# Performance work log

Hardware: AMD Instinct MI355X
Metric: run time of the kernel (lower is better)

Reference implementation:

```python
import jax, jax.numpy as jnp
import numpy as np

INCH, OUTCH, H, W = 1536, 256, 60, 60
B = 4


def resize_bilinear_align_corners(x, oh, ow):
    """F.interpolate(x, (oh, ow), mode='bilinear', align_corners=True) for NCHW x."""
    Bx, C, Hx, Wx = x.shape
    ys = jnp.linspace(0.0, Hx - 1.0, oh)
    xs = jnp.linspace(0.0, Wx - 1.0, ow)
    y0 = jnp.floor(ys).astype(jnp.int32)
    x0 = jnp.floor(xs).astype(jnp.int32)
    y1 = jnp.minimum(y0 + 1, Hx - 1)
    x1 = jnp.minimum(x0 + 1, Wx - 1)
    wy = (ys - y0.astype(x.dtype))[:, None]   # [oh,1]
    wx = (xs - x0.astype(x.dtype))[None, :]   # [1,ow]
    g = lambda yi, xi: x[:, :, yi][:, :, :, xi]  # [B,C,oh,ow]
    top = (1.0 - wx) * g(y0, x0) + wx * g(y0, x1)
    bot = (1.0 - wx) * g(y1, x0) + wx * g(y1, x1)
    return (1.0 - wy) * top + wy * bot


def setup_inputs() -> dict:
    key = jax.random.key(0)
    ks = jax.random.split(key, 8)
    feat_supp = jax.random.normal(ks[0], (B, INCH, H, W), dtype=jnp.float32)
    feat_query = jax.random.normal(ks[1], (B, INCH, H, W), dtype=jnp.float32)
    mask_supp = jax.random.uniform(ks[2], (B, 1, 473, 473), dtype=jnp.float32)
    scale = 0.02
    W_lpf = jax.random.normal(ks[3], (OUTCH, INCH), dtype=jnp.float32) * scale   # shared_LPF 1x1 conv
    W_supp = jax.random.normal(ks[4], (OUTCH, INCH), dtype=jnp.float32) * scale  # supp_linear
    W_query = jax.random.normal(ks[5], (OUTCH, INCH), dtype=jnp.float32) * scale # query_linear
    W_final = jax.random.normal(ks[6], (OUTCH, 2 * OUTCH), dtype=jnp.float32) * scale
    b_final = jax.random.normal(ks[7], (OUTCH,), dtype=jnp.float32) * scale
    return {"feat_supp": feat_supp, "feat_query": feat_query, "mask_supp": mask_supp,
            "W_lpf": W_lpf, "W_supp": W_supp, "W_query": W_query,
            "W_final": W_final, "b_final": b_final}


def conv1x1(x, Wm):
    # x: [b,c,h,w], Wm: [o,c]
    return jnp.einsum('bchw,oc->bohw', x, Wm)


def reference(feat_supp, feat_query, mask_supp, W_lpf, W_supp, W_query, W_final, b_final):
    b, d, h, w = feat_supp.shape
    hw = h * w
    v_supp = conv1x1(feat_supp, W_lpf)    # [b,256,h,w]
    v_query = conv1x1(feat_query, W_lpf)  # [b,256,h,w]
    k = conv1x1(feat_supp, W_supp).transpose(0, 2, 3, 1).reshape(b, hw, -1)   # [b,hw,256]
    q = conv1x1(feat_query, W_query).transpose(0, 2, 3, 1).reshape(b, hw, -1) # [b,hw,256]
    attn = jnp.einsum('bqd,bkd->bqk', q, k)  # [b,hw,hw]
    fg_mask = resize_bilinear_align_corners(mask_supp, h, w)  # [b,1,h,w]
    bg_suppress = ((1.0 - fg_mask) * -999.0).reshape(b, 1, hw)
    attn = jax.nn.softmax(attn + bg_suppress, axis=-1)
    vs = v_supp.transpose(0, 2, 3, 1).reshape(b, hw, -1)      # [b,hw,256]
    out = jnp.einsum('bqk,bkd->bqd', attn, vs)                # [b,hw,256]
    out = out.reshape(b, h, w, -1).transpose(0, 3, 1, 2)      # [b,256,h,w]
    cat = jnp.concatenate([out, v_query], axis=1)             # [b,512,h,w]
    final = jax.nn.relu(conv1x1(cat, W_final) + b_final[None, :, None, None])
    return final, attn.reshape(b, h, w, h, w)
```

## Files before the change

kernel.cpp:

```cpp
#include <hip/hip_runtime.h>
#include <stdint.h>

typedef unsigned short u16;
typedef _Float16 h16;
typedef __attribute__((ext_vector_type(4))) float f32x4;
typedef __attribute__((ext_vector_type(8))) short s16x8;
typedef __attribute__((ext_vector_type(8))) _Float16 h16x8;
typedef __attribute__((ext_vector_type(4))) _Float16 h16x4;
typedef __attribute__((ext_vector_type(4))) unsigned short u16x4;
typedef __attribute__((ext_vector_type(8))) unsigned short u16x8;

#define HW   3600
#define HWP  3648
#define DIM  256
#define CIN  1536
#define LDK  72
#define NCB  58
#define PSH  15.0f

__device__ __forceinline__ u16 f2bf(float f) {
  uint32_t u = __float_as_uint(f);
  uint32_t r = (u + 0x7fffu + ((u >> 16) & 1u)) >> 16;
  return (u16)r;
}
__device__ __forceinline__ float bf2f(u16 h) { return __uint_as_float((uint32_t)h << 16); }

template<int MR, int NR>
__device__ __forceinline__ void mfma_tile(const h16 (*As)[LDK], const h16 (*Bs)[LDK],
                                          int lane, int wr, int wc, f32x4 acc[MR][NR]) {
#pragma unroll
  for (int ks = 0; ks < 2; ++ks) {
    const int ko = ks * 32 + ((lane >> 4) << 3);
    h16x8 af[MR], bv[NR];
#pragma unroll
    for (int m = 0; m < MR; ++m) af[m] = *(const h16x8*)&As[wr + m * 16 + (lane & 15)][ko];
#pragma unroll
    for (int n = 0; n < NR; ++n) bv[n] = *(const h16x8*)&Bs[wc + n * 16 + (lane & 15)][ko];
#pragma unroll
    for (int m = 0; m < MR; ++m)
#pragma unroll
      for (int n = 0; n < NR; ++n)
        acc[m][n] = __builtin_amdgcn_mfma_f32_16x16x32_f16(af[m], bv[n], acc[m][n], 0, 0, 0);
  }
}

template<int MR, int NR>
__device__ __forceinline__ void mfma_tile_bf(const u16 (*As)[LDK], const u16 (*Bs)[LDK],
                                             int lane, int wr, int wc, f32x4 acc[MR][NR]) {
#pragma unroll
  for (int ks = 0; ks < 2; ++ks) {
    const int ko = ks * 32 + ((lane >> 4) << 3);
    s16x8 af[MR], bv[NR];
#pragma unroll
    for (int m = 0; m < MR; ++m) af[m] = *(const s16x8*)&As[wr + m * 16 + (lane & 15)][ko];
#pragma unroll
    for (int n = 0; n < NR; ++n) bv[n] = *(const s16x8*)&Bs[wc + n * 16 + (lane & 15)][ko];
#pragma unroll
    for (int m = 0; m < MR; ++m)
#pragma unroll
      for (int n = 0; n < NR; ++n)
        acc[m][n] = __builtin_amdgcn_mfma_f32_16x16x32_bf16(af[m], bv[n], acc[m][n], 0, 0, 0);
  }
}

#define NW    (256 * 1536)
#define NWF   (256 * 512)
#define NPAD  (4 * 256 * 48)
#define NPREP (14400 + 3 * NW + NWF + NPAD)

__global__ __launch_bounds__(256) void k_prep(
    const float* __restrict__ mask, const float* __restrict__ Wlpf,
    const float* __restrict__ Wsupp, const float* __restrict__ Wquery,
    const float* __restrict__ Wfin,
    float* __restrict__ sup, h16* __restrict__ Wl16, h16* __restrict__ Ws16,
    h16* __restrict__ Wq16, h16* __restrict__ Wf16, u16* __restrict__ vs) {
  int i = blockIdx.x * 256 + threadIdx.x;
  if (i < 14400) {
    int b = i / HW, p = i % HW, py = p / 60, px = p % 60;
    float fg = mask[(size_t)b * 473 * 473 + (size_t)(py * 8) * 473 + px * 8];
    sup[i] = (1.0f - fg) * -999.0f;
  } else if (i < 14400 + NW) {
    int j = i - 14400; Wl16[j] = (h16)Wlpf[j];
  } else if (i < 14400 + 2 * NW) {
    int j = i - 14400 - NW; Ws16[j] = (h16)Wsupp[j];
  } else if (i < 14400 + 3 * NW) {
    int j = i - 14400 - 2 * NW; Wq16[j] = (h16)Wquery[j];
  } else if (i < 14400 + 3 * NW + NWF) {
    int j = i - 14400 - 3 * NW; Wf16[j] = (h16)Wfin[j];
  } else if (i < NPREP) {
    int j = i - 14400 - 3 * NW - NWF;
    int b = j / (256 * 48), rem = j % (256 * 48), d = rem / 48, kk = rem % 48;
    vs[((size_t)b * DIM + d) * HWP + 3600 + kk] = 0;
  }
}

__global__ __launch_bounds__(256) void k_conv(
    const h16* __restrict__ Wl16, const h16* __restrict__ Ws16, const h16* __restrict__ Wq16,
    const float* __restrict__ featS, const float* __restrict__ featQ,
    u16* __restrict__ vs, h16* __restrict__ vq,
    h16* __restrict__ kbuf, h16* __restrict__ qbuf) {
  const int lin = blockIdx.x;
  const int xcd = lin & 7, slot = lin >> 3;
  const int ct = slot >> 2, rb = slot & 3;
  const int b = xcd & 3, isQ = xcd >> 2;
  const int rowBase = rb * 128;
  const int colBase = ct * 128;
  const int tid = threadIdx.x, lane = tid & 63, wid = tid >> 6;
  const int wr = (wid >> 1) << 6, wc = (wid & 1) << 6;
  const bool isV = rowBase < 256;
  const h16* Wbase = isV ? (Wl16 + (size_t)rowBase * CIN)
                         : ((isQ ? Wq16 : Ws16) + (size_t)(rowBase - 256) * CIN);
  const float* feat = (isQ ? featQ : featS) + (size_t)b * CIN * HW;

  __shared__ h16 As[128][LDK];
  __shared__ h16 Bs[128][LDK];
  f32x4 acc[4][4] = {};

  const int a_r = tid >> 3, a_kv = (tid & 7) << 3;
  const int b_n = tid & 127, b_kh = (tid >> 7) << 5;
  const int gnc = colBase + b_n;
  const int gn = gnc < HW ? gnc : HW - 1;

  s16x8 aR[4];
  float bR[32];
#pragma unroll
  for (int i = 0; i < 4; ++i)
    aR[i] = *(const s16x8*)&Wbase[(size_t)(a_r + i * 32) * CIN + a_kv];
#pragma unroll
  for (int g = 0; g < 8; ++g) {
    const float* s = feat + (size_t)(b_kh + g * 4) * HW + gn;
#pragma unroll
    for (int c = 0; c < 4; ++c) bR[g * 4 + c] = s[(size_t)c * HW];
  }

  for (int kt = 0; kt < 24; ++kt) {
#pragma unroll
    for (int i = 0; i < 4; ++i) *(s16x8*)&As[a_r + i * 32][a_kv] = aR[i];
#pragma unroll
    for (int g = 0; g < 8; ++g) {
      h16x4 h = {(h16)bR[g * 4], (h16)bR[g * 4 + 1], (h16)bR[g * 4 + 2], (h16)bR[g * 4 + 3]};
      *(h16x4*)&Bs[b_n][b_kh + g * 4] = h;
    }
    if (kt < 23) {
      const int k0n = (kt + 1) * 64;
#pragma unroll
      for (int i = 0; i < 4; ++i)
        aR[i] = *(const s16x8*)&Wbase[(size_t)(a_r + i * 32) * CIN + k0n + a_kv];
#pragma unroll
      for (int g = 0; g < 8; ++g) {
        const float* s = feat + (size_t)(k0n + b_kh + g * 4) * HW + gn;
#pragma unroll
        for (int c = 0; c < 4; ++c) bR[g * 4 + c] = s[(size_t)c * HW];
      }
    }
    __syncthreads();
    mfma_tile<4, 4>(As, Bs, lane, wr, wc, acc);
    __syncthreads();
  }

  if (isV && !isQ) {
    u16* dst = vs + (size_t)b * DIM * HWP;
#pragma unroll
    for (int m = 0; m < 4; ++m) {
      const int d0 = rowBase + wr + m * 16 + ((lane >> 4) << 2);
#pragma unroll
      for (int n = 0; n < 4; ++n) {
        const int pix = colBase + wc + n * 16 + (lane & 15);
        if (pix < HW) {
#pragma unroll
          for (int r = 0; r < 4; ++r) dst[(size_t)(d0 + r) * HWP + pix] = f2bf(acc[m][n][r]);
        }
      }
    }
  } else {
    h16* dst = (isV ? vq : (isQ ? qbuf : kbuf)) + (size_t)b * HW * DIM;
    const int dOff = isV ? 0 : -256;
#pragma unroll
    for (int m = 0; m < 4; ++m) {
      const int d0 = rowBase + wr + m * 16 + ((lane >> 4) << 2) + dOff;
#pragma unroll
      for (int n = 0; n < 4; ++n) {
        const int pix = colBase + wc + n * 16 + (lane & 15);
        if (pix < HW) {
          h16x4 h = {(h16)acc[m][n][0], (h16)acc[m][n][1],
                     (h16)acc[m][n][2], (h16)acc[m][n][3]};
          *(h16x4*)&dst[(size_t)pix * DIM + d0] = h;
        }
      }
    }
  }
}

__global__ __launch_bounds__(256) void k_qk(
    const h16* __restrict__ qbuf, const h16* __restrict__ kbuf,
    const float* __restrict__ sup, u16* __restrict__ p, float* __restrict__ stat) {
  const int hwid = blockIdx.x;
  const int xcd = hwid & 7, pos = hwid >> 3;
  const int logical = (xcd < 4) ? xcd * 421 + pos : 1684 + (xcd - 4) * 420 + pos;
  const int b = logical / 841, rem = logical % 841;
  const int rt = rem / 29, ct = rem % 29;
  const int rowBase = rt * 128, colBase = ct * 128;
  const int tid = threadIdx.x, lane = tid & 63, wid = tid >> 6;
  const int wr = (wid >> 1) << 6, wc = (wid & 1) << 6;
  const h16* Aq = qbuf + (size_t)b * HW * DIM;
  const h16* Bk = kbuf + (size_t)b * HW * DIM;

  __shared__ __align__(16) char smem[128 * LDK * 2 * 2];
  h16 (*As)[LDK] = (h16(*)[LDK])smem;
  h16 (*Bs)[LDK] = (h16(*)[LDK])(smem + 128 * LDK * 2);
  u16 (*pC)[136] = (u16(*)[136])smem;

  f32x4 acc[4][4] = {};
  const int r0 = tid >> 3, kv8 = (tid & 7) << 3;

  int gaR[4], gbR[4];
#pragma unroll
  for (int i = 0; i < 4; ++i) {
    const int r = r0 + i * 32;
    int ga = rowBase + r; gaR[i] = ga < HW ? ga : HW - 1;
    int gb = colBase + r; gbR[i] = gb < HW ? gb : HW - 1;
  }
  s16x8 aR[4], bR[4];
#pragma unroll
  for (int i = 0; i < 4; ++i) {
    aR[i] = *(const s16x8*)(Aq + (size_t)gaR[i] * DIM + kv8);
    bR[i] = *(const s16x8*)(Bk + (size_t)gbR[i] * DIM + kv8);
  }

  for (int kt = 0; kt < 4; ++kt) {
#pragma unroll
    for (int i = 0; i < 4; ++i) {
      *(s16x8*)&As[r0 + i * 32][kv8] = aR[i];
      *(s16x8*)&Bs[r0 + i * 32][kv8] = bR[i];
    }
    if (kt < 3) {
      const int k0n = (kt + 1) * 64;
#pragma unroll
      for (int i = 0; i < 4; ++i) {
        aR[i] = *(const s16x8*)(Aq + (size_t)gaR[i] * DIM + k0n + kv8);
        bR[i] = *(const s16x8*)(Bk + (size_t)gbR[i] * DIM + k0n + kv8);
      }
    }
    __syncthreads();
    mfma_tile<4, 4>(As, Bs, lane, wr, wc, acc);
    __syncthreads();
  }

  float sup4[4]; int kp4[4];
#pragma unroll
  for (int n = 0; n < 4; ++n) {
    const int kp = colBase + wc + n * 16 + (lane & 15);
    kp4[n] = kp;
    sup4[n] = (kp < HW) ? sup[b * HW + kp] : 0.f;
  }
  float* st = stat + (size_t)(b * NCB + ct * 2 + (wc >> 6)) * HW;
#pragma unroll
  for (int m = 0; m < 4; ++m) {
#pragma unroll
    for (int r = 0; r < 4; ++r) {
      float pr[4];
      float ls = 0.f;
#pragma unroll
      for (int n = 0; n < 4; ++n) {
        pr[n] = (kp4[n] < HW) ? __expf(acc[m][n][r] + sup4[n] - PSH) : 0.f;
        ls += pr[n];
      }
#pragma unroll
      for (int off = 1; off < 16; off <<= 1) ls += __shfl_xor(ls, off);
      const int rl = wr + m * 16 + ((lane >> 4) << 2) + r;
      if ((lane & 15) == 0) {
        const int qp = rowBase + rl;
        if (qp < HW) st[qp] = ls;
      }
#pragma unroll
      for (int n = 0; n < 4; ++n) pC[rl][wc + n * 16 + (lane & 15)] = f2bf(pr[n]);
    }
  }
  __syncthreads();
  u16* pB = p + (size_t)b * HW * HWP;
#pragma unroll
  for (int pass = 0; pass < 8; ++pass) {
    const int rl = pass * 16 + (tid >> 4);
    const int qp = rowBase + rl;
    const int col = colBase + (tid & 15) * 8;
    if (qp < HW && col < HW) {
      u16x8 v = *(const u16x8*)&pC[rl][(tid & 15) * 8];
      *(u16x8*)&pB[(size_t)qp * HWP + col] = v;
    }
  }
}

__global__ __launch_bounds__(256) void k_rowsum(const float* __restrict__ stat,
                                                float* __restrict__ invS) {
  const int i = blockIdx.x * 256 + threadIdx.x;
  if (i >= 4 * HW) return;
  const int b = i / HW, row = i % HW;
  const float* s = stat + (size_t)b * NCB * HW + row;
  float S = 0.f;
  for (int c = 0; c < NCB; ++c) S += s[(size_t)c * HW];
  invS[i] = 1.0f / S;
}

__global__ __launch_bounds__(256) void k_pvsm(
    const u16* __restrict__ p, const u16* __restrict__ vs,
    const float* __restrict__ invS, float* __restrict__ attn, float* __restrict__ part) {
  const int lin = blockIdx.x;
  const int xcd = lin & 7, slot = lin >> 3;
  const int b = xcd >> 1, sphalf = xcd & 1;
  const int split = sphalf * 2 + (slot & 1);
  const int rt = slot >> 1;
  const int rowBase = rt * 64;
  const int tid = threadIdx.x, lane = tid & 63, wid = tid >> 6;
  const int wc = wid << 6;
  const u16* pB = p + (size_t)b * HW * HWP;
  const u16* Bv = vs + (size_t)b * DIM * HWP;
  float* Ab = attn + (size_t)b * HW * HW;

  __shared__ u16 As[64][LDK];
  __shared__ u16 Bs[256][LDK];
  __shared__ float Ir[64];
  f32x4 acc[4][4] = {};

  if (tid < 64) {
    const int ga = rowBase + tid;
    Ir[tid] = (ga < HW) ? invS[b * HW + ga] : 0.f;
  }
  __syncthreads();

  const int a_r = tid >> 4, a_kv = (tid & 15) << 2;
  const int b_r = tid >> 3, b_kv = (tid & 7) << 3;
  const int t0 = split * 15, t1 = (split == 3) ? 57 : split * 15 + 15;

  u16x4 pR[4];
  s16x8 vR[8];
  {
    const int kc = t0 * 64 + a_kv;
#pragma unroll
    for (int i = 0; i < 4; ++i) {
      const int ga = rowBase + a_r + i * 16;
      pR[i] = (u16x4){0, 0, 0, 0};
      if (ga < HW && kc < HW) pR[i] = *(const u16x4*)&pB[(size_t)ga * HWP + kc];
    }
#pragma unroll
    for (int i = 0; i < 8; ++i)
      vR[i] = *(const s16x8*)&Bv[(size_t)(b_r + i * 32) * HWP + t0 * 64 + b_kv];
  }

  for (int kt = t0; kt < t1; ++kt) {
    const int kc = kt * 64 + a_kv;
#pragma unroll
    for (int i = 0; i < 4; ++i) {
      const int r = a_r + i * 16;
      const int ga = rowBase + r;
      if (ga < HW && kc < HW) {
        const float I = Ir[r];
        f32x4 w;
#pragma unroll
        for (int c = 0; c < 4; ++c) w[c] = bf2f(pR[i][c]) * I;
        __builtin_nontemporal_store(w, (f32x4*)(Ab + (size_t)ga * HW + kc));
      }
      *(u16x4*)&As[r][a_kv] = pR[i];
    }
#pragma unroll
    for (int i = 0; i < 8; ++i) *(s16x8*)&Bs[b_r + i * 32][b_kv] = vR[i];
    if (kt + 1 < t1) {
      const int kcn = (kt + 1) * 64 + a_kv;
#pragma unroll
      for (int i = 0; i < 4; ++i) {
        const int ga = rowBase + a_r + i * 16;
        pR[i] = (u16x4){0, 0, 0, 0};
        if (ga < HW && kcn < HW) pR[i] = *(const u16x4*)&pB[(size_t)ga * HWP + kcn];
      }
#pragma unroll
      for (int i = 0; i < 8; ++i)
        vR[i] = *(const s16x8*)&Bv[(size_t)(b_r + i * 32) * HWP + (kt + 1) * 64 + b_kv];
    }
    __syncthreads();
    mfma_tile_bf<4, 4>(As, Bs, lane, 0, wc, acc);
    __syncthreads();
  }
  float* dst = part + (size_t)(split * 4 + b) * HW * DIM;
#pragma unroll
  for (int m = 0; m < 4; ++m) {
    const int pix0 = rowBase + m * 16 + ((lane >> 4) << 2);
#pragma unroll
    for (int n = 0; n < 4; ++n) {
      const int d = wc + n * 16 + (lane & 15);
#pragma unroll
      for (int r = 0; r < 4; ++r)
        if (pix0 + r < HW) dst[(size_t)(pix0 + r) * DIM + d] = acc[m][n][r];
    }
  }
}

__global__ __launch_bounds__(256) void k_pvred(const float* __restrict__ part,
                                               const float* __restrict__ invS,
                                               h16* __restrict__ ov) {
  const size_t idx = (size_t)blockIdx.x * 256 + threadIdx.x;
  const size_t base = idx * 4;
  const size_t stride = (size_t)4 * HW * DIM;
  f32x4 s = *(const f32x4*)&part[base];
#pragma unroll
  for (int sp = 1; sp < 4; ++sp) s += *(const f32x4*)&part[sp * stride + base];
  const float I = invS[base / DIM];
  h16x4 h = {(h16)(s[0] * I), (h16)(s[1] * I), (h16)(s[2] * I), (h16)(s[3] * I)};
  *(h16x4*)&ov[base] = h;
}

__global__ __launch_bounds__(256) void k_final(
    const h16* __restrict__ ov, const h16* __restrict__ vq,
    const h16* __restrict__ Wf16, const float* __restrict__ bfin,
    float* __restrict__ outF) {
  const int tid = threadIdx.x, lane = tid & 63, wid = tid >> 6;
  const int wr = (wid >> 1) << 5, wc = (wid & 1) << 6;
  const int rowBase = blockIdx.x * 64;
  const int colBase = blockIdx.y * 128;
  const int b = blockIdx.z;
  const h16* Aov = ov + (size_t)b * HW * DIM;
  const h16* Avq = vq + (size_t)b * HW * DIM;

  __shared__ h16 As[64][LDK];
  __shared__ h16 Bs[128][LDK];
  f32x4 acc[2][4] = {};

  const int a_r = tid >> 3, a_kv = (tid & 7) << 3;
  int gaR[2];
#pragma unroll
  for (int i = 0; i < 2; ++i) {
    int ga = rowBase + a_r + i * 32; gaR[i] = ga < HW ? ga : HW - 1;
  }

  s16x8 aR[2], bR[4];
#pragma unroll
  for (int i = 0; i < 2; ++i)
    aR[i] = *(const s16x8*)(Aov + (size_t)gaR[i] * DIM + a_kv);
#pragma unroll
  for (int i = 0; i < 4; ++i)
    bR[i] = *(const s16x8*)(Wf16 + (size_t)(colBase + a_r + i * 32) * 512 + a_kv);

  for (int kt = 0; kt < 8; ++kt) {
#pragma unroll
    for (int i = 0; i < 2; ++i) *(s16x8*)&As[a_r + i * 32][a_kv] = aR[i];
#pragma unroll
    for (int i = 0; i < 4; ++i) *(s16x8*)&Bs[a_r + i * 32][a_kv] = bR[i];
    if (kt < 7) {
      const int k0n = (kt + 1) * 64;
      const h16* Asrc = (k0n < 256) ? Aov : Avq;
      const int ak = k0n & 255;
#pragma unroll
      for (int i = 0; i < 2; ++i)
        aR[i] = *(const s16x8*)(Asrc + (size_t)gaR[i] * DIM + ak + a_kv);
#pragma unroll
      for (int i = 0; i < 4; ++i)
        bR[i] = *(const s16x8*)(Wf16 + (size_t)(colBase + a_r + i * 32) * 512 + k0n + a_kv);
    }
    __syncthreads();
    mfma_tile<2, 4>(As, Bs, lane, wr, wc, acc);
    __syncthreads();
  }
  float* dst = outF + (size_t)b * DIM * HW;
#pragma unroll
  for (int n = 0; n < 4; ++n) {
    const int o = colBase + wc + n * 16 + (lane & 15);
    const float bb = bfin[o];
#pragma unroll
    for (int m = 0; m < 2; ++m) {
      const int pix0 = rowBase + wr + m * 16 + ((lane >> 4) << 2);
      if (pix0 < HW) {
        f32x4 v;
#pragma unroll
        for (int r = 0; r < 4; ++r) v[r] = fmaxf(acc[m][n][r] + bb, 0.f);
        *(f32x4*)(dst + (size_t)o * HW + pix0) = v;
      }
    }
  }
}

extern "C" void kernel_launch(void* const* d_in, const int* in_sizes, int n_in,
                              void* d_out, int out_size, void* d_ws, size_t ws_size,
                              hipStream_t stream) {
  (void)in_sizes; (void)n_in; (void)out_size; (void)ws_size;
  const float* featS  = (const float*)d_in[0];
  const float* featQ  = (const float*)d_in[1];
  const float* mask   = (const float*)d_in[2];
  const float* Wlpf   = (const float*)d_in[3];
  const float* Wsupp  = (const float*)d_in[4];
  const float* Wquery = (const float*)d_in[5];
  const float* Wfin   = (const float*)d_in[6];
  const float* bfin   = (const float*)d_in[7];

  float* outF = (float*)d_out;
  float* attn = outF + (size_t)4 * DIM * HW;

  char* w = (char*)d_ws;
  h16* qbuf = (h16*)w;  w += (size_t)4 * HW * DIM * 2;
  h16* kbuf = (h16*)w;  w += (size_t)4 * HW * DIM * 2;
  u16* vs   = (u16*)w;  w += (size_t)4 * DIM * HWP * 2;
  h16* vq   = (h16*)w;  w += (size_t)4 * HW * DIM * 2;
  h16* ov   = (h16*)w;  w += (size_t)4 * HW * DIM * 2;
  float* part = (float*)w;  w += (size_t)4 * 4 * HW * DIM * 4;
  u16* pbuf = (u16*)w;  w += (size_t)4 * HW * HWP * 2;
  h16* Wl16 = (h16*)w;  w += (size_t)NW * 2;
  h16* Ws16 = (h16*)w;  w += (size_t)NW * 2;
  h16* Wq16 = (h16*)w;  w += (size_t)NW * 2;
  h16* Wf16 = (h16*)w;  w += (size_t)NWF * 2;
  float* stat = (float*)w;  w += (size_t)4 * NCB * HW * 4;
  float* invS = (float*)w;  w += (size_t)4 * HW * 4;
  float* sup  = (float*)w;

  k_prep<<<dim3((NPREP + 255) / 256), 256, 0, stream>>>(
      mask, Wlpf, Wsupp, Wquery, Wfin, sup, Wl16, Ws16, Wq16, Wf16, vs);
  k_conv<<<dim3(928), 256, 0, stream>>>(Wl16, Ws16, Wq16, featS, featQ,
                                        vs, vq, kbuf, qbuf);
  k_qk<<<dim3(3364), 256, 0, stream>>>(qbuf, kbuf, sup, pbuf, stat);
  k_rowsum<<<dim3(57), 256, 0, stream>>>(stat, invS);
  k_pvsm<<<dim3(912), 256, 0, stream>>>(pbuf, vs, invS, attn, part);
  k_pvred<<<dim3(3600), 256, 0, stream>>>(part, invS, ov);
  k_final<<<dim3(57, 2, 4), 256, 0, stream>>>(ov, vq, Wf16, bfin, outF);
}
```

Measured before the change: 308.2 us.

## Enlarge conv tile to 256 output rows with 512-thread blocks

```diff
diff --git a/kernel.cpp b/kernel.cpp
--- a/kernel.cpp
+++ b/kernel.cpp
@@ -94,75 +94,66 @@
   }
 }
 
-__global__ __launch_bounds__(256) void k_conv(
+__global__ __launch_bounds__(512, 4) void k_conv(
     const h16* __restrict__ Wl16, const h16* __restrict__ Ws16, const h16* __restrict__ Wq16,
     const float* __restrict__ featS, const float* __restrict__ featQ,
     u16* __restrict__ vs, h16* __restrict__ vq,
     h16* __restrict__ kbuf, h16* __restrict__ qbuf) {
   const int lin = blockIdx.x;
   const int xcd = lin & 7, slot = lin >> 3;
-  const int ct = slot >> 2, rb = slot & 3;
+  const int ct = slot >> 1, rb = slot & 1;
   const int b = xcd & 3, isQ = xcd >> 2;
-  const int rowBase = rb * 128;
   const int colBase = ct * 128;
   const int tid = threadIdx.x, lane = tid & 63, wid = tid >> 6;
   const int wr = (wid >> 1) << 6, wc = (wid & 1) << 6;
-  const bool isV = rowBase < 256;
-  const h16* Wbase = isV ? (Wl16 + (size_t)rowBase * CIN)
-                         : ((isQ ? Wq16 : Ws16) + (size_t)(rowBase - 256) * CIN);
+  const h16* Wsel = (rb == 0) ? Wl16 : (isQ ? Wq16 : Ws16);
   const float* feat = (isQ ? featQ : featS) + (size_t)b * CIN * HW;
 
-  __shared__ h16 As[128][LDK];
+  __shared__ h16 As[256][LDK];
   __shared__ h16 Bs[128][LDK];
   f32x4 acc[4][4] = {};
 
   const int a_r = tid >> 3, a_kv = (tid & 7) << 3;
-  const int b_n = tid & 127, b_kh = (tid >> 7) << 5;
+  const int b_n = tid & 127, b_kh = (tid >> 7) << 4;
   const int gnc = colBase + b_n;
   const int gn = gnc < HW ? gnc : HW - 1;
 
   s16x8 aR[4];
-  float bR[32];
+  float bR[16];
 #pragma unroll
   for (int i = 0; i < 4; ++i)
-    aR[i] = *(const s16x8*)&Wbase[(size_t)(a_r + i * 32) * CIN + a_kv];
-#pragma unroll
-  for (int g = 0; g < 8; ++g) {
-    const float* s = feat + (size_t)(b_kh + g * 4) * HW + gn;
-#pragma unroll
-    for (int c = 0; c < 4; ++c) bR[g * 4 + c] = s[(size_t)c * HW];
-  }
+    aR[i] = *(const s16x8*)&Wsel[(size_t)(a_r + i * 64) * CIN + a_kv];
+#pragma unroll
+  for (int j = 0; j < 16; ++j) bR[j] = feat[(size_t)(b_kh + j) * HW + gn];
 
   for (int kt = 0; kt < 24; ++kt) {
 #pragma unroll
-    for (int i = 0; i < 4; ++i) *(s16x8*)&As[a_r + i * 32][a_kv] = aR[i];
-#pragma unroll
-    for (int g = 0; g < 8; ++g) {
-      h16x4 h = {(h16)bR[g * 4], (h16)bR[g * 4 + 1], (h16)bR[g * 4 + 2], (h16)bR[g * 4 + 3]};
-      *(h16x4*)&Bs[b_n][b_kh + g * 4] = h;
+    for (int i = 0; i < 4; ++i) *(s16x8*)&As[a_r + i * 64][a_kv] = aR[i];
+    {
+      h16x8 h0, h1;
+#pragma unroll
+      for (int c = 0; c < 8; ++c) { h0[c] = (h16)bR[c]; h1[c] = (h16)bR[8 + c]; }
+      *(h16x8*)&Bs[b_n][b_kh] = h0;
+      *(h16x8*)&Bs[b_n][b_kh + 8] = h1;
     }
     if (kt < 23) {
       const int k0n = (kt + 1) * 64;
 #pragma unroll
       for (int i = 0; i < 4; ++i)
-        aR[i] = *(const s16x8*)&Wbase[(size_t)(a_r + i * 32) * CIN + k0n + a_kv];
-#pragma unroll
-      for (int g = 0; g < 8; ++g) {
-        const float* s = feat + (size_t)(k0n + b_kh + g * 4) * HW + gn;
-#pragma unroll
-        for (int c = 0; c < 4; ++c) bR[g * 4 + c] = s[(size_t)c * HW];
-      }
+        aR[i] = *(const s16x8*)&Wsel[(size_t)(a_r + i * 64) * CIN + k0n + a_kv];
+#pragma unroll
+      for (int j = 0; j < 16; ++j) bR[j] = feat[(size_t)(k0n + b_kh + j) * HW + gn];
     }
     __syncthreads();
     mfma_tile<4, 4>(As, Bs, lane, wr, wc, acc);
     __syncthreads();
   }
 
-  if (isV && !isQ) {
+  if (rb == 0 && !isQ) {
     u16* dst = vs + (size_t)b * DIM * HWP;
 #pragma unroll
     for (int m = 0; m < 4; ++m) {
-      const int d0 = rowBase + wr + m * 16 + ((lane >> 4) << 2);
+      const int d0 = wr + m * 16 + ((lane >> 4) << 2);
 #pragma unroll
       for (int n = 0; n < 4; ++n) {
         const int pix = colBase + wc + n * 16 + (lane & 15);
@@ -173,11 +164,10 @@
       }
     }
   } else {
-    h16* dst = (isV ? vq : (isQ ? qbuf : kbuf)) + (size_t)b * HW * DIM;
-    const int dOff = isV ? 0 : -256;
+    h16* dst = ((rb == 0) ? vq : (isQ ? qbuf : kbuf)) + (size_t)b * HW * DIM;
 #pragma unroll
     for (int m = 0; m < 4; ++m) {
-      const int d0 = rowBase + wr + m * 16 + ((lane >> 4) << 2) + dOff;
+      const int d0 = wr + m * 16 + ((lane >> 4) << 2);
 #pragma unroll
       for (int n = 0; n < 4; ++n) {
         const int pix = colBase + wc + n * 16 + (lane & 15);
@@ -510,7 +500,7 @@
 
   k_prep<<<dim3((NPREP + 255) / 256), 256, 0, stream>>>(
       mask, Wlpf, Wsupp, Wquery, Wfin, sup, Wl16, Ws16, Wq16, Wf16, vs);
-  k_conv<<<dim3(928), 256, 0, stream>>>(Wl16, Ws16, Wq16, featS, featQ,
+  k_conv<<<dim3(464), 512, 0, stream>>>(Wl16, Ws16, Wq16, featS, featQ,
                                         vs, vq, kbuf, qbuf);
   k_qk<<<dim3(3364), 256, 0, stream>>>(qbuf, kbuf, sup, pbuf, stat);
   k_rowsum<<<dim3(57), 256, 0, stream>>>(stat, invS);
```

After: 270.5 us. -12.3%, faster.
